# Performance work log

Measured on AMD Instinct MI355X. Metric: run time of the kernel, lower is better.

Reference implementation:

```python
import jax, jax.numpy as jnp
import numpy as np

N_E = 8192
E_DIM = 256
BETA = 0.25


def setup_inputs() -> dict:
    key = jax.random.key(0)
    k1, k2 = jax.random.split(key)
    z = jax.random.normal(k1, (16, E_DIM, 32, 32), dtype=jnp.float32)
    # matches torch init: uniform(-1/n_e, 1/n_e)
    emb_w = jax.random.uniform(k2, (N_E, E_DIM), dtype=jnp.float32,
                               minval=-1.0 / N_E, maxval=1.0 / N_E)
    return {"z": z, "emb_w": emb_w}


def reference(z, emb_w):
    B, C, H, W = z.shape
    zt = jnp.transpose(z, (0, 2, 3, 1))          # b h w c
    zf = zt.reshape(-1, C)                        # [N, e_dim]
    # d[n, k] = ||zf_n||^2 + ||e_k||^2 - 2 zf_n . e_k
    d = (jnp.sum(zf * zf, axis=1, keepdims=True)
         + jnp.sum(emb_w * emb_w, axis=1)
         - 2.0 * jnp.einsum('bd,nd->bn', zf, emb_w))
    idx = jnp.argmin(d, axis=1)                   # [N]
    z_q = emb_w[idx].reshape(zt.shape)            # b h w c
    sg = jax.lax.stop_gradient
    # legacy=True loss
    loss = jnp.mean((sg(z_q) - zt) ** 2) + BETA * jnp.mean((z_q - sg(zt)) ** 2)
    # straight-through estimator
    z_q_st = zt + sg(z_q - zt)
    z_q_out = jnp.transpose(z_q_st, (0, 3, 1, 2))  # b c h w
    return z_q_out, loss, idx.reshape(B, H, W)
```

## Files before the change

kernel.cpp:

```cpp
#include <hip/hip_runtime.h>
#include <math.h>

typedef unsigned int uint;
typedef unsigned short ushort;
typedef unsigned long long u64;
typedef __attribute__((ext_vector_type(8))) short short8;
typedef __attribute__((ext_vector_type(4))) float f32x4;

#define WS_ZT   0ull
#define WS_ZPK  16777216ull
#define WS_EPK  25165824ull
#define WS_SUMZ 29360128ull
#define WS_GMAX 29425664ull
#define WS_BEST 62980096ull
#define WS_LOSS 63111168ull

#define DOT_MARGIN 1.5e-4f

__device__ __forceinline__ ushort f2bf(float f) {
  uint b = __float_as_uint(f);
  b += 0x7fffu + ((b >> 16) & 1u);
  return (ushort)(b >> 16);
}
__device__ __forceinline__ uint ford(float f) {
  uint b = __float_as_uint(f);
  return (b & 0x80000000u) ? ~b : (b | 0x80000000u);
}
__device__ __forceinline__ void gload_lds16(const void* g, void* l) {
  __builtin_amdgcn_global_load_lds(
      (const __attribute__((address_space(1))) unsigned int*)g,
      (__attribute__((address_space(3))) unsigned int*)l, 16, 0, 0);
}

__global__ __launch_bounds__(256) void prep_all(const float* __restrict__ z,
                                                const float* __restrict__ emb,
                                                float* __restrict__ zt,
                                                ushort* __restrict__ zpk,
                                                ushort* __restrict__ epk,
                                                float* __restrict__ sumz) {
  __shared__ float tile[64][65];
  const int bidg = blockIdx.x;
  const int t = threadIdx.x;
  if (bidg < 1024) {
    const int bid = bidg;
    const int kt = bid & 3, hwt = (bid >> 2) & 15, b = bid >> 6;
    const int lane = t & 63, grp = t >> 6;
    const float* src = z + b * 262144 + (kt * 64) * 1024 + hwt * 64;
    for (int kk = grp; kk < 64; kk += 4)
      tile[kk][lane] = src[kk * 1024 + lane];
    __syncthreads();
    for (int rr = grp; rr < 64; rr += 4) {
      const int n = b * 1024 + hwt * 64 + rr;
      zt[n * 256 + kt * 64 + lane] = tile[lane][rr];
    }
    for (int u = t; u < 512; u += 256) {
      const int n_loc = u & 63, kg = u >> 6;
      const int n = b * 1024 + hwt * 64 + n_loc;
      const int k0 = kt * 64 + kg * 8;
      short8 s;
#pragma unroll
      for (int j = 0; j < 8; ++j) s[j] = (short)f2bf(tile[kg * 8 + j][n_loc]);
      *(short8*)(zpk + (size_t)(n >> 4) * 4096 + (k0 >> 5) * 512 +
                 ((k0 >> 3) & 3) * 128 + (n & 15) * 8) = s;
    }
  } else if (bidg < 2048) {
    const int u = (bidg - 1024) * 256 + t;
    const int c = u >> 5, k0 = (u & 31) * 8;
    const float4 v0 = *(const float4*)(emb + c * 256 + k0);
    const float4 v1 = *(const float4*)(emb + c * 256 + k0 + 4);
    short8 s;
    s[0] = (short)f2bf(v0.x); s[1] = (short)f2bf(v0.y);
    s[2] = (short)f2bf(v0.z); s[3] = (short)f2bf(v0.w);
    s[4] = (short)f2bf(v1.x); s[5] = (short)f2bf(v1.y);
    s[6] = (short)f2bf(v1.z); s[7] = (short)f2bf(v1.w);
    *(short8*)(epk + (size_t)(c >> 4) * 4096 + (k0 >> 5) * 512 +
               ((k0 >> 3) & 3) * 128 + (c & 15) * 8) = s;
  } else {
    const int n = ((bidg - 2048) << 8) + t;
    const int b = n >> 10, hw = n & 1023;
    const float* zb = z + b * 262144 + hw;
    float s = 0.f;
#pragma unroll 8
    for (int c = 0; c < 256; ++c) { const float v = zb[c << 10]; s += v * v; }
    sumz[n] = s;
  }
}

__global__ __launch_bounds__(256) void gemm_screen(const ushort* __restrict__ zpk,
                                                   const ushort* __restrict__ epk,
                                                   uint* __restrict__ gmax) {
  __shared__ ushort Cs[16384];
  const int t = threadIdx.x;
  const int w = t >> 6, lane = t & 63;
  const int bid = blockIdx.x;
  const int x = bid & 7, y = bid >> 3;
  const int colb = (y & 15) * 8 + x;
  const int rowg = y >> 4;
  const int n0 = rowg << 10;
  const int m16 = lane & 15, q = lane >> 4;
  const int cix = x * 64 + (y & 15) * 4 + q;

#pragma unroll
  for (int f2 = 0; f2 < 8; ++f2) {
    const int f = w * 8 + f2;
    gload_lds16(epk + (size_t)colb * 16384 + f * 512 + lane * 8, (char*)Cs + f * 1024);
  }

  const ushort* zw = zpk + ((size_t)(n0 >> 4) + w * 4) * 4096 + lane * 8;

  short8 zf[32][4];
#pragma unroll
  for (int v = 0; v < 3; ++v)
#pragma unroll
    for (int jr = 0; jr < 4; ++jr)
      zf[v][jr] = *(const short8*)(zw + ((size_t)((v >> 3) * 16 + jr)) * 4096 +
                                   (v & 7) * 512);
  __syncthreads();

#pragma unroll
  for (int strip = 0; strip < 4; ++strip) {
    const int rbase = n0 + strip * 256 + w * 64;
    f32x4 acc[4][4];
#pragma unroll
    for (int i = 0; i < 4; ++i)
#pragma unroll
      for (int j = 0; j < 4; ++j) acc[i][j] = {0.f, 0.f, 0.f, 0.f};

#pragma unroll
    for (int s32 = 0; s32 < 8; ++s32) {
      const int v = strip * 8 + s32;
      if (v + 3 < 32) {
        const int u = v + 3;
#pragma unroll
        for (int jr = 0; jr < 4; ++jr)
          zf[u][jr] = *(const short8*)(zw + ((size_t)((u >> 3) * 16 + jr)) * 4096 +
                                       (u & 7) * 512);
      }
      short8 cv[4];
#pragma unroll
      for (int ic = 0; ic < 4; ++ic)
        cv[ic] = *(const short8*)&Cs[(size_t)(ic * 8 + s32) * 512 + lane * 8];
#pragma unroll
      for (int ic = 0; ic < 4; ++ic)
#pragma unroll
        for (int jr = 0; jr < 4; ++jr)
          acc[ic][jr] = __builtin_amdgcn_mfma_f32_16x16x32_bf16(cv[ic], zf[v][jr],
                                                                acc[ic][jr], 0, 0, 0);
    }

#pragma unroll
    for (int jr = 0; jr < 4; ++jr) {
      uint pk[4];
#pragma unroll
      for (int ic = 0; ic < 4; ++ic) {
        float m = fmaxf(fmaxf(acc[ic][jr][0], acc[ic][jr][1]),
                        fmaxf(acc[ic][jr][2], acc[ic][jr][3]));
        m = fmaxf(m, __shfl_xor(m, 16, 64));
        const float o = __shfl_xor(m, 32, 64);
        const float glo = (q & 2) ? o : m;
        const float ghi = (q & 2) ? m : o;
        pk[ic] = (uint)f2bf(glo) | ((uint)f2bf(ghi) << 16);
      }
      const uint sv = (q == 0) ? pk[0] : (q == 1) ? pk[1] : (q == 2) ? pk[2] : pk[3];
      gmax[(size_t)(rbase + jr * 16 + m16) * 512 + cix] = sv;
    }
  }
}

__global__ __launch_bounds__(256) void select_rescore(const uint* __restrict__ gmax,
                                                      const float* __restrict__ zt,
                                                      const float* __restrict__ emb,
                                                      const float* __restrict__ sumz,
                                                      u64* __restrict__ best) {
  const int t = threadIdx.x, w = t >> 6, lane = t & 63;
  const int n = (blockIdx.x << 2) + w;
  __shared__ float zrow[4][256];
  __shared__ ushort hits[4][128];
  ((float4*)zrow[w])[lane] = ((const float4*)(zt + (size_t)n * 256))[lane];
  const uint4 r0 = ((const uint4*)(gmax + (size_t)n * 512))[lane];
  const uint4 r1 = ((const uint4*)(gmax + (size_t)n * 512))[lane + 64];
  const uint uv[8] = {r0.x, r0.y, r0.z, r0.w, r1.x, r1.y, r1.z, r1.w};
  float m = -INFINITY;
#pragma unroll
  for (int j = 0; j < 8; ++j) {
    m = fmaxf(m, __uint_as_float(uv[j] << 16));
    m = fmaxf(m, __uint_as_float(uv[j] & 0xffff0000u));
  }
#pragma unroll
  for (int off = 1; off < 64; off <<= 1) m = fmaxf(m, __shfl_xor(m, off, 64));
  const float thr = m - DOT_MARGIN;
  const u64 below = (1ull << lane) - 1ull;
  int base = 0;
#pragma unroll
  for (int j = 0; j < 8; ++j) {
    const int ui = (j < 4) ? lane * 4 + j : 256 + lane * 4 + (j - 4);
    {
      const bool hit = __uint_as_float(uv[j] << 16) >= thr;
      const u64 msk = __ballot(hit);
      if (hit) {
        const int p = base + (int)__popcll(msk & below);
        if (p < 128) hits[w][p] = (ushort)(ui * 2);
      }
      base += (int)__popcll(msk);
    }
    {
      const bool hit = __uint_as_float(uv[j] & 0xffff0000u) >= thr;
      const u64 msk = __ballot(hit);
      if (hit) {
        const int p = base + (int)__popcll(msk & below);
        if (p < 128) hits[w][p] = (ushort)(ui * 2 + 1);
      }
      base += (int)__popcll(msk);
    }
  }
  __threadfence_block();
  int K = base > 128 ? 128 : base;
  const float sz = sumz[n];
  u64 bk = ~0ull;
  for (int id = lane; id < K * 8; id += 64) {
    const int gid = hits[w][id >> 3];
    const int ci = gid >> 1, h = gid & 1;
    const int c = ((ci >> 2) & 15) * 512 + (ci >> 6) * 64 + (ci & 3) * 16 +
                  h * 8 + (id & 7);
    const float4* ea = (const float4*)(emb + c * 256);
    const float4* za = (const float4*)zrow[w];
    float sdot = 0.f, se = 0.f;
#pragma unroll 8
    for (int k = 0; k < 64; ++k) {
      const float4 a = za[k], e = ea[k];
      sdot = fmaf(a.x, e.x, sdot); sdot = fmaf(a.y, e.y, sdot);
      sdot = fmaf(a.z, e.z, sdot); sdot = fmaf(a.w, e.w, sdot);
      se = fmaf(e.x, e.x, se); se = fmaf(e.y, e.y, se);
      se = fmaf(e.z, e.z, se); se = fmaf(e.w, e.w, se);
    }
    const float d = (sz + se) - 2.f * sdot;
    const u64 key = ((u64)ford(d) << 32) | (uint)c;
    if (key < bk) bk = key;
  }
#pragma unroll
  for (int off = 1; off < 64; off <<= 1) {
    const u64 o = (((u64)(uint)__shfl_xor((int)(bk >> 32), off, 64)) << 32) |
                  (uint)__shfl_xor((int)(bk & 0xffffffffu), off, 64);
    if (o < bk) bk = o;
  }
  if (lane == 0) best[n] = bk;
}

__global__ __launch_bounds__(256) void gather_kernel(const float* __restrict__ z,
                                                     const float* __restrict__ emb,
                                                     const u64* __restrict__ best,
                                                     float* __restrict__ out,
                                                     double* __restrict__ loss_acc,
                                                     uint* __restrict__ done) {
  const int t = threadIdx.x;
  const int n0 = blockIdx.x << 6;
  const int n = n0 + (t & 63);
  const int idx = (int)(best[n] & 0xffffffffull);
  const int b_i = n >> 10, hw = n & 1023;
  const int c0 = t >> 6;
  const float* zb = z + b_i * 262144 + hw;
  float* ob = out + b_i * 262144 + hw;
  const float* eb = emb + idx * 256;
  float lsum = 0.f;
#pragma unroll 4
  for (int c = c0; c < 256; c += 4) {
    const float ev = eb[c];
    const float zv = zb[c << 10];
    ob[c << 10] = ev;
    const float d = ev - zv;
    lsum += d * d;
  }
  if (c0 == 0) out[4194305 + n] = (float)idx;
#pragma unroll
  for (int off = 32; off; off >>= 1) lsum += __shfl_down(lsum, off, 64);
  __shared__ double wsum[4];
  if ((t & 63) == 0) wsum[t >> 6] = (double)lsum;
  __syncthreads();
  if (t == 0) {
    atomicAdd(loss_acc, wsum[0] + wsum[1] + wsum[2] + wsum[3]);
    __threadfence();
    if (atomicAdd(done, 1u) == 255u) {
      __threadfence();
      out[4194304] = (float)(1.25 * (*(volatile double*)loss_acc) / 4194304.0);
    }
  }
}

extern "C" void kernel_launch(void* const* d_in, const int* in_sizes, int n_in,
                              void* d_out, int out_size, void* d_ws, size_t ws_size,
                              hipStream_t stream) {
  const float* z = (const float*)d_in[0];
  const float* emb = (const float*)d_in[1];
  float* out = (float*)d_out;
  char* ws = (char*)d_ws;
  float* zt = (float*)(ws + WS_ZT);
  ushort* zpk = (ushort*)(ws + WS_ZPK);
  ushort* epk = (ushort*)(ws + WS_EPK);
  float* sumz = (float*)(ws + WS_SUMZ);
  uint* gmax = (uint*)(ws + WS_GMAX);
  u64* best = (u64*)(ws + WS_BEST);
  double* loss_acc = (double*)(ws + WS_LOSS);
  uint* done = (uint*)(ws + WS_LOSS + 8);

  hipMemsetAsync(ws + WS_LOSS, 0, 16, stream);
  prep_all<<<2112, 256, 0, stream>>>(z, emb, zt, zpk, epk, sumz);
  gemm_screen<<<2048, 256, 0, stream>>>(zpk, epk, gmax);
  select_rescore<<<4096, 256, 0, stream>>>(gmax, zt, emb, sumz, best);
  gather_kernel<<<256, 256, 0, stream>>>(z, emb, best, out, loss_acc, done);
}
```

Measured before the change: 234.1 us.

## Keep half of codebook tile in registers and split gather across channel blocks

The screening GEMM now holds half of the codebook bf16 fragments in registers, loaded once per block, and stages only the other half in LDS. This halves shared memory and adds a launch bound requesting two workgroups per SIMD, aiming at higher occupancy and fewer LDS reads per MFMA step. The cost is much heavier register pressure, with a risk of spills. Separately, the gather kernel is split four ways across channel ranges, giving 1024 blocks instead of 256 to expose more memory parallelism, with the completion counter threshold updated to match.

```diff
diff --git a/kernel.cpp b/kernel.cpp
--- a/kernel.cpp
+++ b/kernel.cpp
@@ -86,10 +86,10 @@
   }
 }
 
-__global__ __launch_bounds__(256) void gemm_screen(const ushort* __restrict__ zpk,
-                                                   const ushort* __restrict__ epk,
-                                                   uint* __restrict__ gmax) {
-  __shared__ ushort Cs[16384];
+__global__ __launch_bounds__(256, 2) void gemm_screen(const ushort* __restrict__ zpk,
+                                                      const ushort* __restrict__ epk,
+                                                      uint* __restrict__ gmax) {
+  __shared__ ushort Cs[8192];
   const int t = threadIdx.x;
   const int w = t >> 6, lane = t & 63;
   const int bid = blockIdx.x;
@@ -100,11 +100,20 @@
   const int m16 = lane & 15, q = lane >> 4;
   const int cix = x * 64 + (y & 15) * 4 + q;
 
-#pragma unroll
-  for (int f2 = 0; f2 < 8; ++f2) {
-    const int f = w * 8 + f2;
-    gload_lds16(epk + (size_t)colb * 16384 + f * 512 + lane * 8, (char*)Cs + f * 1024);
-  }
+  const ushort* ep = epk + (size_t)colb * 16384 + lane * 8;
+
+#pragma unroll
+  for (int f2 = 0; f2 < 4; ++f2) {
+    const int f = w * 4 + f2;
+    gload_lds16(ep + (16 + f) * 512, (char*)Cs + f * 1024);
+  }
+
+  short8 ck[2][8];
+#pragma unroll
+  for (int ic = 0; ic < 2; ++ic)
+#pragma unroll
+    for (int s = 0; s < 8; ++s)
+      ck[ic][s] = *(const short8*)(ep + (ic * 8 + s) * 512);
 
   const ushort* zw = zpk + ((size_t)(n0 >> 4) + w * 4) * 4096 + lane * 8;
 
@@ -136,16 +145,20 @@
           zf[u][jr] = *(const short8*)(zw + ((size_t)((u >> 3) * 16 + jr)) * 4096 +
                                        (u & 7) * 512);
       }
-      short8 cv[4];
-#pragma unroll
-      for (int ic = 0; ic < 4; ++ic)
-        cv[ic] = *(const short8*)&Cs[(size_t)(ic * 8 + s32) * 512 + lane * 8];
-#pragma unroll
-      for (int ic = 0; ic < 4; ++ic)
-#pragma unroll
-        for (int jr = 0; jr < 4; ++jr)
-          acc[ic][jr] = __builtin_amdgcn_mfma_f32_16x16x32_bf16(cv[ic], zf[v][jr],
-                                                                acc[ic][jr], 0, 0, 0);
+      short8 cv2[2];
+      cv2[0] = *(const short8*)&Cs[(size_t)s32 * 512 + lane * 8];
+      cv2[1] = *(const short8*)&Cs[(size_t)(8 + s32) * 512 + lane * 8];
+#pragma unroll
+      for (int jr = 0; jr < 4; ++jr) {
+        acc[0][jr] = __builtin_amdgcn_mfma_f32_16x16x32_bf16(ck[0][s32], zf[v][jr],
+                                                             acc[0][jr], 0, 0, 0);
+        acc[1][jr] = __builtin_amdgcn_mfma_f32_16x16x32_bf16(ck[1][s32], zf[v][jr],
+                                                             acc[1][jr], 0, 0, 0);
+        acc[2][jr] = __builtin_amdgcn_mfma_f32_16x16x32_bf16(cv2[0], zf[v][jr],
+                                                             acc[2][jr], 0, 0, 0);
+        acc[3][jr] = __builtin_amdgcn_mfma_f32_16x16x32_bf16(cv2[1], zf[v][jr],
+                                                             acc[3][jr], 0, 0, 0);
+      }
     }
 
 #pragma unroll
@@ -253,24 +266,25 @@
                                                      double* __restrict__ loss_acc,
                                                      uint* __restrict__ done) {
   const int t = threadIdx.x;
-  const int n0 = blockIdx.x << 6;
-  const int n = n0 + (t & 63);
+  const int bid = blockIdx.x;
+  const int n = ((bid >> 2) << 6) + (t & 63);
+  const int cc = bid & 3;
   const int idx = (int)(best[n] & 0xffffffffull);
   const int b_i = n >> 10, hw = n & 1023;
-  const int c0 = t >> 6;
+  const int c0 = cc * 64 + (t >> 6);
   const float* zb = z + b_i * 262144 + hw;
   float* ob = out + b_i * 262144 + hw;
   const float* eb = emb + idx * 256;
   float lsum = 0.f;
 #pragma unroll 4
-  for (int c = c0; c < 256; c += 4) {
+  for (int c = c0; c < cc * 64 + 64; c += 4) {
     const float ev = eb[c];
     const float zv = zb[c << 10];
     ob[c << 10] = ev;
     const float d = ev - zv;
     lsum += d * d;
   }
-  if (c0 == 0) out[4194305 + n] = (float)idx;
+  if (cc == 0 && (t >> 6) == 0) out[4194305 + n] = (float)idx;
 #pragma unroll
   for (int off = 32; off; off >>= 1) lsum += __shfl_down(lsum, off, 64);
   __shared__ double wsum[4];
@@ -279,7 +293,7 @@
   if (t == 0) {
     atomicAdd(loss_acc, wsum[0] + wsum[1] + wsum[2] + wsum[3]);
     __threadfence();
-    if (atomicAdd(done, 1u) == 255u) {
+    if (atomicAdd(done, 1u) == 1023u) {
       __threadfence();
       out[4194304] = (float)(1.25 * (*(volatile double*)loss_acc) / 4194304.0);
     }
@@ -306,5 +320,5 @@
   prep_all<<<2112, 256, 0, stream>>>(z, emb, zt, zpk, epk, sumz);
   gemm_screen<<<2048, 256, 0, stream>>>(zpk, epk, gmax);
   select_rescore<<<4096, 256, 0, stream>>>(gmax, zt, emb, sumz, best);
-  gather_kernel<<<256, 256, 0, stream>>>(z, emb, best, out, loss_acc, done);
-}
+  gather_kernel<<<1024, 256, 0, stream>>>(z, emb, best, out, loss_acc, done);
+}
```

New measurement: 265.2 us. 1.13x slower.
